# Optimization experiments

Hardware: AMD Instinct MI355X
Metric: run time of the kernel (lower is better)

## Reference

```python
import jax, jax.numpy as jnp
import numpy as np

B, S, D, H = 8, 2048, 1024, 16
HD = D // H  # head_dim = 64


def setup_inputs() -> dict:
    key = jax.random.key(0)
    ks = jax.random.split(key, 10)
    s = 0.02
    return {
        "x": jax.random.normal(ks[0], (B, S, D), jnp.float32),
        "mask": jnp.zeros((B, 1, S), jnp.float32),
        "Wq": jax.random.normal(ks[1], (D, D), jnp.float32) * s,
        "bq": jnp.zeros((D,), jnp.float32),
        "Wk": jax.random.normal(ks[2], (D, D), jnp.float32) * s,
        "bk": jnp.zeros((D,), jnp.float32),
        "Wv": jax.random.normal(ks[3], (D, D), jnp.float32) * s,
        "bv": jnp.zeros((D,), jnp.float32),
        "wa": jax.random.normal(ks[4], (HD, 1), jnp.float32) * s,
        "ba": jnp.zeros((1,), jnp.float32),
        "wb": jax.random.normal(ks[5], (HD, 1), jnp.float32) * s,
        "bb": jnp.zeros((1,), jnp.float32),
        "Wu": jax.random.normal(ks[6], (HD, HD), jnp.float32) * s,
        "bu": jnp.zeros((HD,), jnp.float32),
        "Wo": jax.random.normal(ks[7], (D, D), jnp.float32) * s,
        "bo": jnp.zeros((D,), jnp.float32),
        "gamma": jnp.ones((D,), jnp.float32),
        "beta_ln": jnp.zeros((D,), jnp.float32),
    }


def _split_heads(t):
    # [B,S,D] -> [B,H,S,HD]
    return t.reshape(B, S, H, HD).transpose(0, 2, 1, 3)


def reference(x, mask, Wq, bq, Wk, bk, Wv, bv, wa, ba, wb, bb, Wu, bu, Wo, bo, gamma, beta_ln):
    scale = 1.0 / jnp.sqrt(jnp.float32(HD))
    q = _split_heads(x @ Wq + bq)  # [B,H,S,HD]
    k = _split_heads(x @ Wk + bk)
    v = _split_heads(x @ Wv + bv)

    # additive attention over queries -> global query vector per head
    alphascore = (jnp.squeeze(q @ wa, -1) + ba[0]) * scale + mask  # [B,H,S]
    alphaw = jax.nn.softmax(alphascore, axis=-1)
    q_av = jnp.einsum('bhs,bhsd->bhd', alphaw, q)

    p = k * q_av[:, :, None, :]  # gated keys [B,H,S,HD]
    betascore = (jnp.squeeze(p @ wb, -1) + bb[0]) * scale + mask
    betaw = jax.nn.softmax(betascore, axis=-1)
    p_av = jnp.einsum('bhs,bhsd->bhd', betaw, p)

    u = v * p_av[:, :, None, :]  # gated values
    r = u @ Wu + bu  # [B,H,S,HD]
    newr = (r + q).transpose(0, 2, 1, 3).reshape(B, S, D)
    attn_out = newr @ Wo + bo

    h = x + attn_out
    mu = jnp.mean(h, axis=-1, keepdims=True)
    var = jnp.mean(jnp.square(h - mu), axis=-1, keepdims=True)
    return (h - mu) * jax.lax.rsqrt(var + 1e-6) * gamma + beta_ln
```

## Files before the change

kernel.cpp:

```cpp
#include <hip/hip_runtime.h>
#include <cstdint>

#define BB 8
#define SS 2048
#define DD 1024
#define HH 16
#define HDIM 64
#define MTOT (BB*SS)
#define QKVW 2048

typedef __attribute__((ext_vector_type(8))) __bf16 bf16x8;
typedef __attribute__((ext_vector_type(4))) float f32x4;

#define AS1(p) ((const __attribute__((address_space(1))) void*)(p))
#define AS3(p) ((__attribute__((address_space(3))) void*)(p))

__device__ __forceinline__ float bf2f(uint16_t u){
  return __uint_as_float(((uint32_t)u) << 16);
}
__device__ __forceinline__ uint16_t f2bf(float f){
  uint32_t u = __float_as_uint(f);
  return (uint16_t)((u + 0x7fffu + ((u >> 16) & 1u)) >> 16);
}

__global__ __launch_bounds__(256)
void k_prep(const float* __restrict__ x,
            const float* __restrict__ Wq, const float* __restrict__ Wk,
            const float* __restrict__ Wv, const float* __restrict__ Wo,
            const float* __restrict__ bq, const float* __restrict__ bv,
            uint16_t* __restrict__ xb, uint16_t* __restrict__ Wt,
            uint16_t* __restrict__ Wkt, uint16_t* __restrict__ WoT,
            float* __restrict__ bqv)
{
  __shared__ float t[32][33];
  const int blk = blockIdx.x, tid = threadIdx.x;
  if (blk < 2048){
    const int n4 = MTOT*DD/4;
    for (int i = blk*256 + tid; i < n4; i += 2048*256){
      float4 v = reinterpret_cast<const float4*>(x)[i];
      ushort4 o;
      o.x = f2bf(v.x); o.y = f2bf(v.y); o.z = f2bf(v.z); o.w = f2bf(v.w);
      reinterpret_cast<ushort4*>(xb)[i] = o;
    }
  } else if (blk < 6144){
    const int zb = blk - 2048;
    const int z = zb >> 10, rem = zb & 1023;
    const int by = rem >> 5, bx = rem & 31;
    const float* src = (z==0)?Wq:(z==1)?Wv:(z==2)?Wk:Wo;
    uint16_t* dst = (z==0)?Wt:(z==1)?(Wt + 1024*1024):(z==2)?Wkt:WoT;
    const int k0 = by*32, n0 = bx*32;
    const int tx = tid & 31, ty = tid >> 5;
    #pragma unroll
    for (int r = 0; r < 4; ++r)
      t[ty + r*8][tx] = src[(size_t)(k0 + ty + r*8)*1024 + n0 + tx];
    __syncthreads();
    #pragma unroll
    for (int r = 0; r < 4; ++r)
      dst[(size_t)(n0 + ty + r*8)*1024 + k0 + tx] = f2bf(t[tx][ty + r*8]);
  } else {
    const int i = (blk - 6144)*256 + tid;
    if (i < QKVW)
      bqv[i] = (i < 1024) ? bq[i] : bv[i-1024];
  }
}

#define BARRIER __builtin_amdgcn_s_barrier()

#define READA(BUF, MH) { \
  const uint16_t* _sl = lds + ((BUF)*4 + (MH))*8192; \
  _Pragma("unroll") \
  for (int f = 0; f < 4; ++f) \
    _Pragma("unroll") \
    for (int ks = 0; ks < 2; ++ks) \
      a[f][ks] = *(const bf16x8*)(_sl + (wm*64 + f*16 + l15)*64 + (((ks*4 + l4) ^ l7)<<3)); \
}

#define READB(BUF, NH, BV) { \
  const uint16_t* _sl = lds + ((BUF)*4 + 2 + (NH))*8192; \
  _Pragma("unroll") \
  for (int j = 0; j < 2; ++j) \
    _Pragma("unroll") \
    for (int ks = 0; ks < 2; ++ks) \
      BV[j][ks] = *(const bf16x8*)(_sl + (wn*32 + j*16 + l15)*64 + (((ks*4 + l4) ^ l7)<<3)); \
}

#define MMA(MH, NH, BV) { \
  __builtin_amdgcn_s_setprio(1); \
  _Pragma("unroll") \
  for (int ks = 0; ks < 2; ++ks) \
    _Pragma("unroll") \
    for (int f = 0; f < 4; ++f) \
      _Pragma("unroll") \
      for (int j = 0; j < 2; ++j) \
        acc[(MH)*4+f][(NH)*2+j] = __builtin_amdgcn_mfma_f32_16x16x32_bf16(a[f][ks], BV[j][ks], acc[(MH)*4+f][(NH)*2+j], 0, 0, 0); \
  __builtin_amdgcn_s_setprio(0); }

#define STAGEA(T, H) { \
  char* _d = (char*)lds + ((((T)&1)*4 + (H))*16384) + wave*1024; \
  _Pragma("unroll") \
  for (int l = 0; l < 2; ++l) \
    __builtin_amdgcn_global_load_lds(AS1(pA + (l*131072 + (H)*65536 + (T)*64)), AS3(_d + l*8192), 16, 0, 0); \
}

#define STAGEB(T, H) { \
  char* _d = (char*)lds + ((((T)&1)*4 + 2 + (H))*16384) + wave*1024; \
  _Pragma("unroll") \
  for (int l = 0; l < 2; ++l) \
    __builtin_amdgcn_global_load_lds(AS1(pB + (l*131072 + (H)*32768 + (T)*64)), AS3(_d + l*8192), 16, 0, 0); \
}

template<int EPI, int NB_T>
__global__ __launch_bounds__(512)
void k_gemm256(const uint16_t* __restrict__ A, const uint16_t* __restrict__ Bt,
               const float* __restrict__ bias, const uint16_t* __restrict__ resid16,
               uint16_t* __restrict__ Cout,
               const float* __restrict__ waP, const float* __restrict__ baP,
               const float* __restrict__ maskP,
               float* __restrict__ cpartA, float* __restrict__ dpartA)
{
  constexpr int N = NB_T * 256;
  __shared__ uint16_t lds[8 * 8192];
  const int tid = threadIdx.x;
  const int lane = tid & 63, wave = tid >> 6;
  const int wm = wave >> 2, wn = wave & 3;
  const int l15 = lane & 15, l4 = lane >> 4, l7 = lane & 7;

  const int nwg = gridDim.x, cpx = nwg >> 3, bid = blockIdx.x;
  const int wg = (bid & 7) * cpx + (bid >> 3);
  const int m0 = (wg / NB_T) << 8, n0 = (wg % NB_T) << 8;

  const int colbase = (((tid & 7) ^ ((tid >> 3) & 7)) << 3);
  const uint16_t* pA = A  + (size_t)(m0 + (tid >> 3)) * 1024 + colbase;
  const uint16_t* pB = Bt + (size_t)(n0 + ((tid >> 8) << 6) + ((tid >> 3) & 31)) * 1024 + colbase;

  f32x4 acc[8][4] = {};
  bf16x8 a[4][2], b0[2][2], b1[2][2];

  STAGEA(0,0); STAGEB(0,1); STAGEA(0,1); STAGEB(0,0);
  STAGEA(1,0); STAGEB(1,1); STAGEA(1,1);
  asm volatile("s_waitcnt vmcnt(6)" ::: "memory");
  BARRIER;

  #pragma unroll
  for (int I = 0; I < 7; ++I){
    const int e = 2*I;
    READA(0,0); READB(0,0,b0); STAGEB(e+1, 0);
    BARRIER; MMA(0,0,b0); BARRIER;
    READB(0,1,b1); STAGEA(e+2, 0);
    BARRIER; MMA(0,1,b1); BARRIER;
    READA(0,1); STAGEB(e+2, 1);
    BARRIER; MMA(1,1,b1); BARRIER;
    STAGEA(e+2, 1);
    asm volatile("s_waitcnt vmcnt(6)" ::: "memory");
    BARRIER; MMA(1,0,b0); BARRIER;
    READA(1,0); READB(1,0,b0); STAGEB(e+2, 0);
    BARRIER; MMA(0,0,b0); BARRIER;
    READB(1,1,b1); STAGEA(e+3, 0);
    BARRIER; MMA(0,1,b1); BARRIER;
    READA(1,1); STAGEB(e+3, 1);
    BARRIER; MMA(1,1,b1); BARRIER;
    STAGEA(e+3, 1);
    asm volatile("s_waitcnt vmcnt(6)" ::: "memory");
    BARRIER; MMA(1,0,b0); BARRIER;
  }

  {
    READA(0,0); READB(0,0,b0); STAGEB(15, 0);
    BARRIER; MMA(0,0,b0); BARRIER;
    READB(0,1,b1);
    BARRIER; MMA(0,1,b1); BARRIER;
    READA(0,1);
    BARRIER; MMA(1,1,b1); BARRIER;
    asm volatile("s_waitcnt vmcnt(0)" ::: "memory");
    BARRIER; MMA(1,0,b0); BARRIER;
    READA(1,0); READB(1,0,b0);
    BARRIER; MMA(0,0,b0); BARRIER;
    READB(1,1,b1);
    BARRIER; MMA(0,1,b1); BARRIER;
    READA(1,1);
    BARRIER; MMA(1,1,b1); BARRIER;
    MMA(1,0,b0);
  }

  #pragma unroll
  for (int mh = 0; mh < 2; ++mh)
  #pragma unroll
  for (int f = 0; f < 4; ++f)
  #pragma unroll
  for (int nh = 0; nh < 2; ++nh)
  #pragma unroll
  for (int j = 0; j < 2; ++j){
    const int gcol = n0 + wn*64 + nh*32 + j*16 + l15;
    const float bi = bias[gcol];
    const int rbase = m0 + wm*128 + mh*64 + f*16 + l4*4;
    #pragma unroll
    for (int rr = 0; rr < 4; ++rr){
      const size_t idx = (size_t)(rbase + rr)*N + gcol;
      float v = acc[mh*4+f][nh*2+j][rr] + bi;
      if (EPI == 1) v += bf2f(resid16[idx]);
      Cout[idx] = f2bf(v);
    }
  }

  if (EPI == 0 && n0 < 1024){
    const int hg = (n0 >> 6) + wn;
    const float bav = baP[0];
    float bcol[2][2], wv[2][2];
    #pragma unroll
    for (int nh = 0; nh < 2; ++nh)
    #pragma unroll
    for (int j = 0; j < 2; ++j){
      const int c = nh*32 + j*16 + l15;
      bcol[nh][j] = bias[n0 + wn*64 + c];
      wv[nh][j]   = waP[c];
    }
    float colacc[2][2] = {{0.f,0.f},{0.f,0.f}};
    float esum = 0.f;
    #pragma unroll
    for (int mh = 0; mh < 2; ++mh)
    #pragma unroll
    for (int f = 0; f < 4; ++f)
    #pragma unroll
    for (int rr = 0; rr < 4; ++rr){
      float qv[2][2];
      float p = 0.f;
      #pragma unroll
      for (int nh = 0; nh < 2; ++nh)
      #pragma unroll
      for (int j = 0; j < 2; ++j){
        qv[nh][j] = acc[mh*4+f][nh*2+j][rr] + bcol[nh][j];
        p += qv[nh][j] * wv[nh][j];
      }
      p += __shfl_xor(p, 1); p += __shfl_xor(p, 2);
      p += __shfl_xor(p, 4); p += __shfl_xor(p, 8);
      const int grow = m0 + wm*128 + mh*64 + f*16 + l4*4 + rr;
      const float E = __expf((p + bav)*0.125f + maskP[grow]);
      esum += E;
      #pragma unroll
      for (int nh = 0; nh < 2; ++nh)
      #pragma unroll
      for (int j = 0; j < 2; ++j)
        colacc[nh][j] += E * qv[nh][j];
    }
    const int rb = (m0 >> 7) + wm;
    #pragma unroll
    for (int nh = 0; nh < 2; ++nh)
    #pragma unroll
    for (int j = 0; j < 2; ++j){
      float v = colacc[nh][j];
      v += __shfl_xor(v, 16); v += __shfl_xor(v, 32);
      if (l4 == 0)
        cpartA[(size_t)rb*1024 + n0 + wn*64 + nh*32 + j*16 + l15] = v;
    }
    esum += __shfl_xor(esum, 16); esum += __shfl_xor(esum, 32);
    if (lane == 0) dpartA[rb*16 + hg] = esum;
  }
}

__global__ __launch_bounds__(256)
void k_mergeA(const float* __restrict__ cpartA, const float* __restrict__ dpartA,
              const float* __restrict__ wb,
              float* __restrict__ qavB, float* __restrict__ wvecB)
{
  __shared__ float dsum[16];
  const int blk = blockIdx.x, tid = threadIdx.x;
  const int b = blk >> 2, c = (blk & 3)*256 + tid;
  if (tid < 16){
    float d = 0.f;
    #pragma unroll
    for (int rb = 0; rb < 16; ++rb) d += dpartA[(b*16 + rb)*16 + tid];
    dsum[tid] = d;
  }
  __syncthreads();
  float s = 0.f;
  #pragma unroll
  for (int rb = 0; rb < 16; ++rb) s += cpartA[(size_t)(b*16 + rb)*1024 + c];
  const float qv = s / dsum[(c >> 6) & 15];
  qavB[b*1024 + c]  = qv;
  wvecB[b*1024 + c] = qv * wb[c & 63];
}

__global__ __launch_bounds__(256)
void k_foldB(const uint16_t* __restrict__ Wkt, const float* __restrict__ wvecB,
             const float* __restrict__ bk, const float* __restrict__ bbP,
             uint16_t* __restrict__ pBb, float* __restrict__ csB)
{
  __shared__ float wl[64];
  __shared__ float redc[64];
  const int bh = blockIdx.x, b = bh >> 4, h = bh & 15;
  const int tid = threadIdx.x;
  if (tid < 64) wl[tid] = wvecB[b*1024 + h*64 + tid];
  __syncthreads();
  const int k0 = tid*4;
  float a0 = 0.f, a1 = 0.f, a2 = 0.f, a3 = 0.f;
  for (int d = 0; d < 64; ++d){
    const float w = wl[d];
    const ushort4 r = *(const ushort4*)(Wkt + (size_t)(h*64 + d)*1024 + k0);
    a0 += bf2f(r.x)*w; a1 += bf2f(r.y)*w; a2 += bf2f(r.z)*w; a3 += bf2f(r.w)*w;
  }
  uint16_t* dst = pBb + (size_t)bh*1024 + k0;
  dst[0] = f2bf(a0); dst[1] = f2bf(a1); dst[2] = f2bf(a2); dst[3] = f2bf(a3);
  if (tid < 64) redc[tid] = bk[h*64 + tid] * wl[tid];
  __syncthreads();
  if (tid == 0){
    float s = 0.f;
    for (int i = 0; i < 64; ++i) s += redc[i];
    csB[bh] = s + bbP[0];
  }
}

__global__ __launch_bounds__(256)
void k_scoreM(const uint16_t* __restrict__ xb, const uint16_t* __restrict__ pBb,
              const float* __restrict__ csB, const float* __restrict__ mask,
              float* __restrict__ EB, float* __restrict__ dpartB)
{
  __shared__ float sred[4][16];
  __shared__ float csl[16];
  const int blk = blockIdx.x, tid = threadIdx.x;
  const int b = blk >> 5;
  const int wave = tid >> 6, lane = tid & 63;
  const int l15 = lane & 15, l4 = lane >> 4;
  if (tid < 16) csl[tid] = csB[b*16 + tid];
  __syncthreads();
  const int row0 = blk*64 + wave*16;
  const uint16_t* pa = xb  + (size_t)(row0 + l15)*1024 + l4*8;
  const uint16_t* pb = pBb + (size_t)(b*16 + l15)*1024 + l4*8;

  f32x4 acc = {};
  #pragma unroll
  for (int kk = 0; kk < 32; ++kk){
    const bf16x8 af = *(const bf16x8*)(pa + kk*32);
    const bf16x8 bf = *(const bf16x8*)(pb + kk*32);
    acc = __builtin_amdgcn_mfma_f32_16x16x32_bf16(af, bf, acc, 0, 0, 0);
  }
  float es = 0.f;
  #pragma unroll
  for (int r = 0; r < 4; ++r){
    const int row = row0 + l4*4 + r;
    const float E = __expf((acc[r] + csl[l15])*0.125f + mask[row]);
    EB[(size_t)row*16 + l15] = E;
    es += E;
  }
  es += __shfl_xor(es, 16); es += __shfl_xor(es, 32);
  if (l4 == 0) sred[wave][l15] = es;
  __syncthreads();
  if (tid < 16)
    dpartB[blk*16 + tid] = sred[0][tid] + sred[1][tid] + sred[2][tid] + sred[3][tid];
}

__global__ __launch_bounds__(256)
void k_xsumV(const uint16_t* __restrict__ xb, const float* __restrict__ EB,
             float* __restrict__ xwp)
{
  const int blk = blockIdx.x, tid = threadIdx.x;
  const int row0 = blk*64;
  const int c0 = tid*4;
  float acc[16][4];
  #pragma unroll
  for (int h = 0; h < 16; ++h){
    #pragma unroll
    for (int c = 0; c < 4; ++c) acc[h][c] = 0.f;
  }
  for (int r = 0; r < 64; ++r){
    const int row = row0 + r;
    const ushort4 xv4 = *(const ushort4*)(xb + (size_t)row*1024 + c0);
    const float x0 = bf2f(xv4.x), x1 = bf2f(xv4.y), x2 = bf2f(xv4.z), x3 = bf2f(xv4.w);
    const float4* e4 = (const float4*)(EB + (size_t)row*16);
    const float4 e0 = e4[0], e1 = e4[1], e2 = e4[2], e3 = e4[3];
    #define ACCH(hh, ee) { acc[hh][0] += x0*(ee); acc[hh][1] += x1*(ee); \
                           acc[hh][2] += x2*(ee); acc[hh][3] += x3*(ee); }
    ACCH(0,  e0.x) ACCH(1,  e0.y) ACCH(2,  e0.z) ACCH(3,  e0.w)
    ACCH(4,  e1.x) ACCH(5,  e1.y) ACCH(6,  e1.z) ACCH(7,  e1.w)
    ACCH(8,  e2.x) ACCH(9,  e2.y) ACCH(10, e2.z) ACCH(11, e2.w)
    ACCH(12, e3.x) ACCH(13, e3.y) ACCH(14, e3.z) ACCH(15, e3.w)
    #undef ACCH
  }
  float* dst = xwp + (size_t)blk*16*1024;
  #pragma unroll
  for (int h = 0; h < 16; ++h)
    *(float4*)(dst + h*1024 + c0) =
        (float4){acc[h][0], acc[h][1], acc[h][2], acc[h][3]};
}

__global__ __launch_bounds__(512)
void k_finalB(const float* __restrict__ xwp, const float* __restrict__ dpartB,
              const float* __restrict__ qavB, const uint16_t* __restrict__ Wkt,
              const float* __restrict__ bk, const float* __restrict__ Wu,
              uint16_t* __restrict__ WuPT)
{
  __shared__ float xwl[1024];
  __shared__ float kvl[64];
  __shared__ float pavl[64];
  __shared__ float dsh;
  const int bh = blockIdx.x, b = bh >> 4, h = bh & 15;
  const int tid = threadIdx.x;
  #pragma unroll
  for (int i = 0; i < 2; ++i){
    const int idx = i*512 + tid;
    float s = 0.f;
    #pragma unroll
    for (int rc = 0; rc < 32; ++rc)
      s += xwp[((size_t)(b*32 + rc)*16 + h)*1024 + idx];
    xwl[idx] = s;
  }
  if (tid < 32){
    float d = dpartB[(b*32 + tid)*16 + h];
    d += __shfl_xor(d, 1); d += __shfl_xor(d, 2); d += __shfl_xor(d, 4);
    d += __shfl_xor(d, 8); d += __shfl_xor(d, 16);
    if (tid == 0) dsh = d;
  }
  __syncthreads();
  const int d = tid >> 3, q = tid & 7;
  const uint16_t* wrow = Wkt + (size_t)(h*64 + d)*1024 + q*128;
  const float* xwq = xwl + q*128;
  float s = 0.f;
  #pragma unroll
  for (int i = 0; i < 16; ++i){
    const bf16x8 v = *(const bf16x8*)(wrow + i*8);
    #pragma unroll
    for (int e = 0; e < 8; ++e) s += (float)v[e]*xwq[i*8+e];
  }
  s += __shfl_xor(s, 1); s += __shfl_xor(s, 2); s += __shfl_xor(s, 4);
  if (q == 0) kvl[d] = s;
  __syncthreads();
  if (tid < 64)
    pavl[tid] = qavB[b*1024 + h*64 + tid] * (kvl[tid]/dsh + bk[h*64 + tid]);
  __syncthreads();
  uint16_t* dst = WuPT + (size_t)bh*4096;
  for (int idx = tid; idx < 4096; idx += 512){
    const int i = idx & 63, jcol = idx >> 6;
    dst[idx] = f2bf(pavl[i]*Wu[i*64 + jcol]);
  }
}

__global__ __launch_bounds__(256)
void k_newr(const uint16_t* __restrict__ qkv, const uint16_t* __restrict__ WuPT,
            const float* __restrict__ bu, uint16_t* __restrict__ newr)
{
  const int bh = blockIdx.x >> 3, st = blockIdx.x & 7;
  const int b = bh >> 4, h = bh & 15;
  const int tid = threadIdx.x, wave = tid >> 6, lane = tid & 63;
  const int l15 = lane & 15, l4 = lane >> 4;
  const int s0 = st*256 + wave*64;
  const uint16_t* vb = qkv + 1024 + h*64;
  const uint16_t* wt = WuPT + (size_t)bh*4096;

  f32x4 acc[4][4] = {};
  #pragma unroll
  for (int ks = 0; ks < 2; ++ks){
    bf16x8 bfr[4];
    #pragma unroll
    for (int n = 0; n < 4; ++n)
      bfr[n] = *(const bf16x8*)(wt + (n*16 + l15)*64 + ks*32 + l4*8);
    #pragma unroll
    for (int m = 0; m < 4; ++m){
      const int s = s0 + m*16 + l15;
      bf16x8 af = *(const bf16x8*)(vb + (size_t)(b*SS + s)*QKVW + ks*32 + l4*8);
      #pragma unroll
      for (int n = 0; n < 4; ++n)
        acc[m][n] = __builtin_amdgcn_mfma_f32_16x16x32_bf16(af, bfr[n], acc[m][n], 0, 0, 0);
    }
  }
  #pragma unroll
  for (int n = 0; n < 4; ++n){
    const int j = n*16 + l15;
    const float bj = bu[j];
    #pragma unroll
    for (int m = 0; m < 4; ++m){
      #pragma unroll
      for (int r = 0; r < 4; ++r){
        const int s = s0 + m*16 + l4*4 + r;
        const size_t qidx = (size_t)(b*SS + s)*QKVW + h*64 + j;
        const float q = bf2f(qkv[qidx]);
        newr[(size_t)(b*SS + s)*DD + h*64 + j] = f2bf(acc[m][n][r] + bj + q);
      }
    }
  }
}

__global__ __launch_bounds__(256)
void k_ln(const uint16_t* __restrict__ h16, const float* __restrict__ gamma,
          const float* __restrict__ beta, float* __restrict__ out)
{
  __shared__ float r1[256], r2[256];
  const int row = blockIdx.x, tid = threadIdx.x;
  const ushort4 hv = ((const ushort4*)(h16 + (size_t)row*DD))[tid];
  float v0 = bf2f(hv.x), v1 = bf2f(hv.y), v2 = bf2f(hv.z), v3 = bf2f(hv.w);
  float s  = v0 + v1 + v2 + v3;
  float ss = v0*v0 + v1*v1 + v2*v2 + v3*v3;
  r1[tid] = s; r2[tid] = ss; __syncthreads();
  for (int off = 128; off > 0; off >>= 1){
    if (tid < off){ r1[tid] += r1[tid+off]; r2[tid] += r2[tid+off]; }
    __syncthreads();
  }
  const float mu  = r1[0]*(1.f/1024.f);
  const float var = r2[0]*(1.f/1024.f) - mu*mu;
  const float inv = rsqrtf(var + 1e-6f);
  const float4 g  = ((const float4*)gamma)[tid];
  const float4 be = ((const float4*)beta)[tid];
  float4 o;
  o.x = (v0-mu)*inv*g.x + be.x;
  o.y = (v1-mu)*inv*g.y + be.y;
  o.z = (v2-mu)*inv*g.z + be.z;
  o.w = (v3-mu)*inv*g.w + be.w;
  ((float4*)(out + (size_t)row*DD))[tid] = o;
}

extern "C" void kernel_launch(void* const* d_in, const int* in_sizes, int n_in,
                              void* d_out, int out_size, void* d_ws, size_t ws_size,
                              hipStream_t stream) {
  const float* x    = (const float*)d_in[0];
  const float* mask = (const float*)d_in[1];
  const float* Wq   = (const float*)d_in[2];
  const float* bq   = (const float*)d_in[3];
  const float* Wk   = (const float*)d_in[4];
  const float* bk   = (const float*)d_in[5];
  const float* Wv   = (const float*)d_in[6];
  const float* bv   = (const float*)d_in[7];
  const float* wa   = (const float*)d_in[8];
  const float* ba   = (const float*)d_in[9];
  const float* wb   = (const float*)d_in[10];
  const float* bb   = (const float*)d_in[11];
  const float* Wu   = (const float*)d_in[12];
  const float* bu   = (const float*)d_in[13];
  const float* Wo   = (const float*)d_in[14];
  const float* bo   = (const float*)d_in[15];
  const float* gamma= (const float*)d_in[16];
  const float* beta = (const float*)d_in[17];
  float* out = (float*)d_out;

  char* ws = (char*)d_ws;
  const size_t MB = 1ull << 20;
  uint16_t* xb    = (uint16_t*)(ws);
  uint16_t* Wt    = (uint16_t*)(ws + 32*MB);
  uint16_t* Wkt   = (uint16_t*)(ws + 36*MB);
  uint16_t* WoT   = (uint16_t*)(ws + 38*MB);
  float*    bqv   = (float*)   (ws + 40*MB);
  uint16_t* WuPT  = (uint16_t*)(ws + 41*MB);
  uint16_t* qkv   = (uint16_t*)(ws + 42*MB);
  uint16_t* hbuf16= (uint16_t*)(ws + 42*MB);
  float* cpartA = (float*)(ws + 110*MB);
  float* dpartA = (float*)(ws + 111*MB);
  float* qavB   = (float*)(ws + 112*MB);
  float* wvecB  = (float*)(ws + 113*MB);
  uint16_t* pBb = (uint16_t*)(ws + 114*MB);
  float* csB    = (float*)(ws + 115*MB);
  float* EB     = (float*)(ws + 116*MB);
  float* dpartB = (float*)(ws + 118*MB);
  float* xwp    = (float*)(ws + 119*MB);
  uint16_t* newr= (uint16_t*)(ws + 138*MB);

  k_prep<<<6156, 256, 0, stream>>>(x, Wq, Wk, Wv, Wo, bq, bv, xb, Wt, Wkt, WoT, bqv);

  k_gemm256<0,8><<<(MTOT/256)*(QKVW/256), 512, 0, stream>>>(
      xb, Wt, bqv, nullptr, qkv, wa, ba, mask, cpartA, dpartA);

  k_mergeA<<<32, 256, 0, stream>>>(cpartA, dpartA, wb, qavB, wvecB);
  k_foldB<<<128, 256, 0, stream>>>(Wkt, wvecB, bk, bb, pBb, csB);
  k_scoreM<<<256, 256, 0, stream>>>(xb, pBb, csB, mask, EB, dpartB);
  k_xsumV<<<256, 256, 0, stream>>>(xb, EB, xwp);
  k_finalB<<<128, 512, 0, stream>>>(xwp, dpartB, qavB, Wkt, bk, Wu, WuPT);

  k_newr<<<BB*HH*8, 256, 0, stream>>>(qkv, WuPT, bu, newr);
  k_gemm256<1,4><<<(MTOT/256)*(DD/256), 512, 0, stream>>>(
      newr, WoT, bo, xb, hbuf16, nullptr, nullptr, nullptr, nullptr, nullptr);
  k_ln<<<MTOT, 256, 0, stream>>>(hbuf16, gamma, beta, out);
}
```

Measured before the change: 221.2 us.

## Fuse merge/fold and score/xsum kernels to cut launches and intermediate traffic

Merges the qav merge kernel into the fold kernel, with each block recomputing its head's qav slice. Also fuses the beta-score MFMA kernel with the x-weighted-sum kernel so the exponentiated scores stay in shared memory instead of going through a global buffer. The fused score kernel uses 512 threads, each handling 2 columns, with only 4 waves doing the score MFMAs. This removes two launches and the EB/wvecB round trips, but during the score phase half the waves sit idle and each block now does more serial work.

Result: faster. 216.9 us (median of 2 runs) (-2.0%).

```diff
diff --git a/kernel.cpp b/kernel.cpp
--- a/kernel.cpp
+++ b/kernel.cpp
@@ -258,44 +258,35 @@
 }
 
 __global__ __launch_bounds__(256)
-void k_mergeA(const float* __restrict__ cpartA, const float* __restrict__ dpartA,
-              const float* __restrict__ wb,
-              float* __restrict__ qavB, float* __restrict__ wvecB)
-{
-  __shared__ float dsum[16];
-  const int blk = blockIdx.x, tid = threadIdx.x;
-  const int b = blk >> 2, c = (blk & 3)*256 + tid;
-  if (tid < 16){
-    float d = 0.f;
-    #pragma unroll
-    for (int rb = 0; rb < 16; ++rb) d += dpartA[(b*16 + rb)*16 + tid];
-    dsum[tid] = d;
-  }
-  __syncthreads();
-  float s = 0.f;
-  #pragma unroll
-  for (int rb = 0; rb < 16; ++rb) s += cpartA[(size_t)(b*16 + rb)*1024 + c];
-  const float qv = s / dsum[(c >> 6) & 15];
-  qavB[b*1024 + c]  = qv;
-  wvecB[b*1024 + c] = qv * wb[c & 63];
-}
-
-__global__ __launch_bounds__(256)
-void k_foldB(const uint16_t* __restrict__ Wkt, const float* __restrict__ wvecB,
-             const float* __restrict__ bk, const float* __restrict__ bbP,
-             uint16_t* __restrict__ pBb, float* __restrict__ csB)
+void k_mergefold(const float* __restrict__ cpartA, const float* __restrict__ dpartA,
+                 const float* __restrict__ wb, const uint16_t* __restrict__ Wkt,
+                 const float* __restrict__ bk, const float* __restrict__ bbP,
+                 float* __restrict__ qavB, uint16_t* __restrict__ pBb,
+                 float* __restrict__ csB)
 {
   __shared__ float wl[64];
   __shared__ float redc[64];
   const int bh = blockIdx.x, b = bh >> 4, h = bh & 15;
   const int tid = threadIdx.x;
-  if (tid < 64) wl[tid] = wvecB[b*1024 + h*64 + tid];
+  if (tid < 64){
+    float s = 0.f;
+    #pragma unroll
+    for (int rb = 0; rb < 16; ++rb)
+      s += cpartA[(size_t)(b*16 + rb)*1024 + h*64 + tid];
+    float d = 0.f;
+    #pragma unroll
+    for (int rb = 0; rb < 16; ++rb)
+      d += dpartA[(b*16 + rb)*16 + h];
+    const float qv = s / d;
+    qavB[b*1024 + h*64 + tid] = qv;
+    wl[tid] = qv * wb[tid];
+  }
   __syncthreads();
   const int k0 = tid*4;
   float a0 = 0.f, a1 = 0.f, a2 = 0.f, a3 = 0.f;
-  for (int d = 0; d < 64; ++d){
-    const float w = wl[d];
-    const ushort4 r = *(const ushort4*)(Wkt + (size_t)(h*64 + d)*1024 + k0);
+  for (int d2 = 0; d2 < 64; ++d2){
+    const float w = wl[d2];
+    const ushort4 r = *(const ushort4*)(Wkt + (size_t)(h*64 + d2)*1024 + k0);
     a0 += bf2f(r.x)*w; a1 += bf2f(r.y)*w; a2 += bf2f(r.z)*w; a3 += bf2f(r.w)*w;
   }
   uint16_t* dst = pBb + (size_t)bh*1024 + k0;
@@ -309,11 +300,12 @@
   }
 }
 
-__global__ __launch_bounds__(256)
-void k_scoreM(const uint16_t* __restrict__ xb, const uint16_t* __restrict__ pBb,
-              const float* __restrict__ csB, const float* __restrict__ mask,
-              float* __restrict__ EB, float* __restrict__ dpartB)
-{
+__global__ __launch_bounds__(512)
+void k_scoreXsum(const uint16_t* __restrict__ xb, const uint16_t* __restrict__ pBb,
+                 const float* __restrict__ csB, const float* __restrict__ mask,
+                 float* __restrict__ xwp, float* __restrict__ dpartB)
+{
+  __shared__ float el[64][16];
   __shared__ float sred[4][16];
   __shared__ float csl[16];
   const int blk = blockIdx.x, tid = threadIdx.x;
@@ -322,64 +314,67 @@
   const int l15 = lane & 15, l4 = lane >> 4;
   if (tid < 16) csl[tid] = csB[b*16 + tid];
   __syncthreads();
-  const int row0 = blk*64 + wave*16;
-  const uint16_t* pa = xb  + (size_t)(row0 + l15)*1024 + l4*8;
-  const uint16_t* pb = pBb + (size_t)(b*16 + l15)*1024 + l4*8;
-
-  f32x4 acc = {};
-  #pragma unroll
-  for (int kk = 0; kk < 32; ++kk){
-    const bf16x8 af = *(const bf16x8*)(pa + kk*32);
-    const bf16x8 bf = *(const bf16x8*)(pb + kk*32);
-    acc = __builtin_amdgcn_mfma_f32_16x16x32_bf16(af, bf, acc, 0, 0, 0);
-  }
-  float es = 0.f;
-  #pragma unroll
-  for (int r = 0; r < 4; ++r){
-    const int row = row0 + l4*4 + r;
-    const float E = __expf((acc[r] + csl[l15])*0.125f + mask[row]);
-    EB[(size_t)row*16 + l15] = E;
-    es += E;
-  }
-  es += __shfl_xor(es, 16); es += __shfl_xor(es, 32);
-  if (l4 == 0) sred[wave][l15] = es;
+  const int row0 = blk*64;
+
+  if (wave < 4){
+    const int rw = row0 + wave*16;
+    const uint16_t* pa = xb  + (size_t)(rw + l15)*1024 + l4*8;
+    const uint16_t* pb = pBb + (size_t)(b*16 + l15)*1024 + l4*8;
+    f32x4 acc = {};
+    #pragma unroll
+    for (int kk = 0; kk < 32; ++kk){
+      const bf16x8 af = *(const bf16x8*)(pa + kk*32);
+      const bf16x8 bf = *(const bf16x8*)(pb + kk*32);
+      acc = __builtin_amdgcn_mfma_f32_16x16x32_bf16(af, bf, acc, 0, 0, 0);
+    }
+    float es = 0.f;
+    #pragma unroll
+    for (int r = 0; r < 4; ++r){
+      const int rloc = wave*16 + l4*4 + r;
+      const float E = __expf((acc[r] + csl[l15])*0.125f + mask[row0 + rloc]);
+      el[rloc][l15] = E;
+      es += E;
+    }
+    es += __shfl_xor(es, 16); es += __shfl_xor(es, 32);
+    if (l4 == 0) sred[wave][l15] = es;
+  }
   __syncthreads();
   if (tid < 16)
     dpartB[blk*16 + tid] = sred[0][tid] + sred[1][tid] + sred[2][tid] + sred[3][tid];
-}
-
-__global__ __launch_bounds__(256)
-void k_xsumV(const uint16_t* __restrict__ xb, const float* __restrict__ EB,
-             float* __restrict__ xwp)
-{
-  const int blk = blockIdx.x, tid = threadIdx.x;
-  const int row0 = blk*64;
-  const int c0 = tid*4;
-  float acc[16][4];
-  #pragma unroll
-  for (int h = 0; h < 16; ++h){
-    #pragma unroll
-    for (int c = 0; c < 4; ++c) acc[h][c] = 0.f;
-  }
+
+  const int c0 = tid*2;
+  float acc0[16], acc1[16];
+  #pragma unroll
+  for (int h = 0; h < 16; ++h){ acc0[h] = 0.f; acc1[h] = 0.f; }
   for (int r = 0; r < 64; ++r){
-    const int row = row0 + r;
-    const ushort4 xv4 = *(const ushort4*)(xb + (size_t)row*1024 + c0);
-    const float x0 = bf2f(xv4.x), x1 = bf2f(xv4.y), x2 = bf2f(xv4.z), x3 = bf2f(xv4.w);
-    const float4* e4 = (const float4*)(EB + (size_t)row*16);
-    const float4 e0 = e4[0], e1 = e4[1], e2 = e4[2], e3 = e4[3];
-    #define ACCH(hh, ee) { acc[hh][0] += x0*(ee); acc[hh][1] += x1*(ee); \
-                           acc[hh][2] += x2*(ee); acc[hh][3] += x3*(ee); }
-    ACCH(0,  e0.x) ACCH(1,  e0.y) ACCH(2,  e0.z) ACCH(3,  e0.w)
-    ACCH(4,  e1.x) ACCH(5,  e1.y) ACCH(6,  e1.z) ACCH(7,  e1.w)
-    ACCH(8,  e2.x) ACCH(9,  e2.y) ACCH(10, e2.z) ACCH(11, e2.w)
-    ACCH(12, e3.x) ACCH(13, e3.y) ACCH(14, e3.z) ACCH(15, e3.w)
-    #undef ACCH
+    const uint32_t xv = *(const uint32_t*)(xb + (size_t)(row0 + r)*1024 + c0);
+    const float x0 = __uint_as_float(xv << 16);
+    const float x1 = __uint_as_float(xv & 0xffff0000u);
+    const float4 e0 = *(const float4*)(&el[r][0]);
+    const float4 e1 = *(const float4*)(&el[r][4]);
+    const float4 e2 = *(const float4*)(&el[r][8]);
+    const float4 e3 = *(const float4*)(&el[r][12]);
+    acc0[0]  += x0*e0.x; acc1[0]  += x1*e0.x;
+    acc0[1]  += x0*e0.y; acc1[1]  += x1*e0.y;
+    acc0[2]  += x0*e0.z; acc1[2]  += x1*e0.z;
+    acc0[3]  += x0*e0.w; acc1[3]  += x1*e0.w;
+    acc0[4]  += x0*e1.x; acc1[4]  += x1*e1.x;
+    acc0[5]  += x0*e1.y; acc1[5]  += x1*e1.y;
+    acc0[6]  += x0*e1.z; acc1[6]  += x1*e1.z;
+    acc0[7]  += x0*e1.w; acc1[7]  += x1*e1.w;
+    acc0[8]  += x0*e2.x; acc1[8]  += x1*e2.x;
+    acc0[9]  += x0*e2.y; acc1[9]  += x1*e2.y;
+    acc0[10] += x0*e2.z; acc1[10] += x1*e2.z;
+    acc0[11] += x0*e2.w; acc1[11] += x1*e2.w;
+    acc0[12] += x0*e3.x; acc1[12] += x1*e3.x;
+    acc0[13] += x0*e3.y; acc1[13] += x1*e3.y;
+    acc0[14] += x0*e3.z; acc1[14] += x1*e3.z;
+    acc0[15] += x0*e3.w; acc1[15] += x1*e3.w;
   }
   float* dst = xwp + (size_t)blk*16*1024;
   #pragma unroll
   for (int h = 0; h < 16; ++h)
-    *(float4*)(dst + h*1024 + c0) =
-        (float4){acc[h][0], acc[h][1], acc[h][2], acc[h][3]};
+    *(float2*)(dst + h*1024 + c0) = (float2){acc0[h], acc1[h]};
 }
 
 __global__ __launch_bounds__(512)
@@ -542,10 +537,8 @@
   float* cpartA = (float*)(ws + 110*MB);
   float* dpartA = (float*)(ws + 111*MB);
   float* qavB   = (float*)(ws + 112*MB);
-  float* wvecB  = (float*)(ws + 113*MB);
   uint16_t* pBb = (uint16_t*)(ws + 114*MB);
   float* csB    = (float*)(ws + 115*MB);
-  float* EB     = (float*)(ws + 116*MB);
   float* dpartB = (float*)(ws + 118*MB);
   float* xwp    = (float*)(ws + 119*MB);
   uint16_t* newr= (uint16_t*)(ws + 138*MB);
@@ -555,10 +548,8 @@
   k_gemm256<0,8><<<(MTOT/256)*(QKVW/256), 512, 0, stream>>>(
       xb, Wt, bqv, nullptr, qkv, wa, ba, mask, cpartA, dpartA);
 
-  k_mergeA<<<32, 256, 0, stream>>>(cpartA, dpartA, wb, qavB, wvecB);
-  k_foldB<<<128, 256, 0, stream>>>(Wkt, wvecB, bk, bb, pBb, csB);
-  k_scoreM<<<256, 256, 0, stream>>>(xb, pBb, csB, mask, EB, dpartB);
-  k_xsumV<<<256, 256, 0, stream>>>(xb, EB, xwp);
+  k_mergefold<<<128, 256, 0, stream>>>(cpartA, dpartA, wb, Wkt, bk, bb, qavB, pBb, csB);
+  k_scoreXsum<<<256, 512, 0, stream>>>(xb, pBb, csB, mask, xwp, dpartB);
   k_finalB<<<128, 512, 0, stream>>>(xwp, dpartB, qavB, Wkt, bk, Wu, WuPT);
 
   k_newr<<<BB*HH*8, 256, 0, stream>>>(qkv, WuPT, bu, newr);
```
